# Kernel optimization log

Hardware: AMD Instinct MI355X
Metric: run time of the kernel (lower is better)

Reference implementation:

```python
import jax, jax.numpy as jnp
import numpy as np

B, S, D, H, DH = 4, 2048, 1024, 16, 64


def setup_inputs() -> dict:
    key = jax.random.key(0)
    ks = jax.random.split(key, 12)
    inp = {
        "query": jax.random.normal(ks[0], (B, S, D), jnp.float32),
        "key": jax.random.normal(ks[1], (B, S, D), jnp.float32),
        "value": jax.random.normal(ks[2], (B, S, D), jnp.float32),
        # causal mask, broadcast over batch and heads
        "mask": jnp.tril(jnp.ones((S, S), jnp.int32))[None, None, :, :],
        "Wq": jax.random.normal(ks[3], (D, D), jnp.float32) * 0.02,
        "bq": jnp.zeros((D,), jnp.float32),
        "Wk": jax.random.normal(ks[4], (D, D), jnp.float32) * 0.02,
        "bk": jnp.zeros((D,), jnp.float32),
        "Wv": jax.random.normal(ks[5], (D, D), jnp.float32) * 0.02,
        "bv": jnp.zeros((D,), jnp.float32),
        "Wo": jax.random.normal(ks[6], (D, D), jnp.float32) * 0.02,
        "bo": jnp.zeros((D,), jnp.float32),
    }
    return inp


def reference(query, key, value, mask, Wq, bq, Wk, bk, Wv, bv, Wo, bo):
    # linear projections (torch Linear: x @ W^T + b; here W stored as [in, out])
    q = query @ Wq + bq
    k = key @ Wk + bk
    v = value @ Wv + bv
    # [B, S, D] -> [B, H, S, DH]
    q = q.reshape(B, S, H, DH).transpose(0, 2, 1, 3)
    k = k.reshape(B, S, H, DH).transpose(0, 2, 1, 3)
    v = v.reshape(B, S, H, DH).transpose(0, 2, 1, 3)
    # materialized O(S^2) attention scores
    scores = jnp.einsum("bhqd,bhkd->bhqk", q, k) * (DH ** -0.5)
    scores = jnp.where(mask == 0, jnp.float32(-jnp.inf), scores)
    attn = jax.nn.softmax(scores, axis=-1)  # dropout is identity in eval
    x = jnp.einsum("bhqk,bhkd->bhqd", attn, v)
    # [B, H, S, DH] -> [B, S, D]
    x = x.transpose(0, 2, 1, 3).reshape(B, S, D)
    out = x @ Wo + bo
    return out
```

## Files before the change

kernel.cpp:

```cpp
#include <hip/hip_runtime.h>
#include <hip/hip_bf16.h>


typedef __bf16 bf16x8 __attribute__((ext_vector_type(8)));
typedef float f32x4 __attribute__((ext_vector_type(4)));

#define GLOBAL_AS __attribute__((address_space(1)))
#define LDS_AS __attribute__((address_space(3)))

#if __has_builtin(__builtin_amdgcn_exp2f)
#define EXP2(x) __builtin_amdgcn_exp2f(x)
#else
#define EXP2(x) __expf((x) * 0.6931471805599453f)
#endif
#define QSCALE 0.18033688f

static __device__ __forceinline__ unsigned short f2bf(float f) {
    __bf16 h = (__bf16)f;
    return __builtin_bit_cast(unsigned short, h);
}

static __device__ __forceinline__ void gload_lds16(const void* g, void* l) {
    __builtin_amdgcn_global_load_lds((const GLOBAL_AS void*)g, (LDS_AS void*)l, 16, 0, 0);
}

__global__ __launch_bounds__(256) void cvt3(const float* __restrict__ q,
                                            const float* __restrict__ k,
                                            const float* __restrict__ v,
                                            unsigned short* __restrict__ dq,
                                            unsigned short* __restrict__ dk,
                                            unsigned short* __restrict__ dv, int n8) {
    const int z = blockIdx.z;
    const float* src = (z == 0) ? q : (z == 1) ? k : v;
    unsigned short* dst = (z == 0) ? dq : (z == 1) ? dk : dv;
    int i = blockIdx.x * 256 + threadIdx.x;
    if (i >= n8) return;
    const float4* s = (const float4*)src + 2 * (size_t)i;
    float4 v0 = s[0], v1 = s[1];
    unsigned short h[8] = {f2bf(v0.x), f2bf(v0.y), f2bf(v0.z), f2bf(v0.w),
                           f2bf(v1.x), f2bf(v1.y), f2bf(v1.z), f2bf(v1.w)};
    *(uint4*)(dst + 8 * (size_t)i) = *(const uint4*)h;
}

__global__ void transpose_weights(const float* __restrict__ W0, const float* __restrict__ W1,
                                  const float* __restrict__ W2, const float* __restrict__ W3,
                                  unsigned short* __restrict__ T0, unsigned short* __restrict__ T1,
                                  unsigned short* __restrict__ T2, unsigned short* __restrict__ T3) {
    const float* W; unsigned short* T;
    switch (blockIdx.z) { case 0: W=W0; T=T0; break; case 1: W=W1; T=T1; break;
                          case 2: W=W2; T=T2; break; default: W=W3; T=T3; }
    __shared__ float tile[32][33];
    int tx = threadIdx.x, ty = threadIdx.y;
    int k0 = blockIdx.x * 32, n0 = blockIdx.y * 32;
#pragma unroll
    for (int j = 0; j < 4; j++) tile[ty + 8*j][tx] = W[(size_t)(k0 + ty + 8*j) * 1024 + n0 + tx];
    __syncthreads();
#pragma unroll
    for (int j = 0; j < 4; j++) T[(size_t)(n0 + ty + 8*j) * 1024 + k0 + tx] = f2bf(tile[tx][ty + 8*j]);
}

static __device__ __forceinline__ void gemm_core(const unsigned short* __restrict__ A,
                                                 const unsigned short* __restrict__ BT,
                                                 unsigned short* Asm, unsigned short* Bsm,
                                                 int rowBase, int colBase, int t,
                                                 f32x4 acc[4][4]) {
    const int lane = t & 63, w = t >> 6;
    const int g = lane >> 4, r16 = lane & 15;
    const int wr = w >> 1, wc = w & 1;
    const int K = 1024;
    const int srow = t >> 3;
    const int scol = ((t & 7) ^ ((t >> 3) & 7)) * 8;

    const unsigned short* srcA[4];
    const unsigned short* srcB[4];
#pragma unroll
    for (int j = 0; j < 4; j++) {
        srcA[j] = A  + (size_t)(rowBase + srow + 32 * j) * K + scol;
        srcB[j] = BT + (size_t)(colBase + srow + 32 * j) * K + scol;
    }
    unsigned short* dstA = Asm + 512 * w;
    unsigned short* dstB = Bsm + 512 * w;

#pragma unroll
    for (int j = 0; j < 4; j++) {
        gload_lds16(srcA[j], dstA + 2048 * j);
        gload_lds16(srcB[j], dstB + 2048 * j);
    }
    __syncthreads();

    int cur = 0;
    for (int k0 = 0; k0 < K; k0 += 64) {
        if (k0 + 64 < K) {
            unsigned short* dA = dstA + (cur ^ 1) * 8192;
            unsigned short* dB = dstB + (cur ^ 1) * 8192;
#pragma unroll
            for (int j = 0; j < 4; j++) {
                gload_lds16(srcA[j] + k0 + 64, dA + 2048 * j);
                gload_lds16(srcB[j] + k0 + 64, dB + 2048 * j);
            }
        }
        const unsigned short* As = Asm + cur * 8192;
        const unsigned short* Bs = Bsm + cur * 8192;
#pragma unroll
        for (int ks = 0; ks < 2; ks++) {
            bf16x8 a[4], b[4];
#pragma unroll
            for (int m = 0; m < 4; m++) {
                int row = 64 * wr + 16 * m + r16;
                a[m] = *(const bf16x8*)(As + row * 64 + ((4 * ks + g) ^ (row & 7)) * 8);
            }
#pragma unroll
            for (int n = 0; n < 4; n++) {
                int row = 64 * wc + 16 * n + r16;
                b[n] = *(const bf16x8*)(Bs + row * 64 + ((4 * ks + g) ^ (row & 7)) * 8);
            }
#pragma unroll
            for (int m = 0; m < 4; m++)
#pragma unroll
                for (int n = 0; n < 4; n++)
                    acc[m][n] = __builtin_amdgcn_mfma_f32_16x16x32_bf16(a[m], b[n], acc[m][n], 0, 0, 0);
        }
        __syncthreads();
        cur ^= 1;
    }
}

__global__ __launch_bounds__(256) void gemm_qkv(
        const unsigned short* __restrict__ Xq, const unsigned short* __restrict__ Xk,
        const unsigned short* __restrict__ Xv,
        const unsigned short* __restrict__ WTq, const unsigned short* __restrict__ WTk,
        const unsigned short* __restrict__ WTv,
        const float* __restrict__ bq, const float* __restrict__ bk, const float* __restrict__ bv,
        unsigned short* __restrict__ Qb, unsigned short* __restrict__ Kb,
        unsigned short* __restrict__ VT) {
    __shared__ alignas(16) unsigned short smem[32768];
    unsigned short* Asm = smem;
    unsigned short* Bsm = smem + 16384;
    const int z = blockIdx.z;
    const unsigned short* A  = (z == 0) ? Xq : (z == 1) ? Xk : Xv;
    const unsigned short* BT = (z == 0) ? WTq : (z == 1) ? WTk : WTv;
    const float* bias        = (z == 0) ? bq : (z == 1) ? bk : bv;
    const int rowBase = blockIdx.y * 128, colBase = blockIdx.x * 128;
    const int t = threadIdx.x;
    const int lane = t & 63, w = t >> 6;
    const int g = lane >> 4, r16 = lane & 15;
    const int wr = w >> 1, wc = w & 1;

    f32x4 acc[4][4] = {};
    gemm_core(A, BT, Asm, Bsm, rowBase, colBase, t, acc);

    float bv4[4];
#pragma unroll
    for (int n = 0; n < 4; n++) bv4[n] = bias[colBase + 64 * wc + 16 * n + r16];

    if (z == 2) {
        const int TS = 136;
        unsigned short* Tsm = smem;
#pragma unroll
        for (int m = 0; m < 4; m++) {
#pragma unroll
            for (int n = 0; n < 4; n++) {
                int c = 64 * wc + 16 * n + r16;
                int r = 64 * wr + 16 * m + 4 * g;
                unsigned short pk[4];
#pragma unroll
                for (int i = 0; i < 4; i++) pk[i] = f2bf(acc[m][n][i] + bv4[n]);
                *(uint2*)(Tsm + c * TS + r) = *(const uint2*)pk;
            }
        }
        __syncthreads();
        const int bidx = rowBase >> 11;
        const int sBase = rowBase & 2047;
        const int sloc = (t & 15) * 8;
#pragma unroll
        for (int jj = 0; jj < 8; jj++) {
            int dloc = (t >> 4) + 16 * jj;
            uint4 v = *(const uint4*)(Tsm + dloc * TS + sloc);
            int col = colBase + dloc;
            int hidx = col >> 6, dh = col & 63;
            *(uint4*)&VT[(((size_t)(bidx * 16 + hidx)) * 64 + dh) * 2048 + sBase + sloc] = v;
        }
    } else {
#pragma unroll
        for (int m = 0; m < 4; m++) {
#pragma unroll
            for (int n = 0; n < 4; n++) {
#pragma unroll
                for (int i = 0; i < 4; i++) {
                    int row = rowBase + 64 * wr + 16 * m + 4 * g + i;
                    int col = colBase + 64 * wc + 16 * n + r16;
                    float v = acc[m][n][i] + bv4[n];
                    int bidx = row >> 11, s = row & 2047;
                    int hidx = col >> 6, dh = col & 63;
                    size_t bh = (size_t)(bidx * 16 + hidx);
                    if (z == 0) Qb[(bh * 2048 + s) * 64 + dh] = f2bf(v * QSCALE);
                    else        Kb[(bh * 2048 + s) * 64 + dh] = f2bf(v);
                }
            }
        }
    }
}

__global__ __launch_bounds__(256) void gemm_out(const unsigned short* __restrict__ A,
                                                const unsigned short* __restrict__ BT,
                                                const float* __restrict__ bias,
                                                float* __restrict__ Out) {
    __shared__ alignas(16) unsigned short smem[32768];
    unsigned short* Asm = smem;
    unsigned short* Bsm = smem + 16384;
    const int rowBase = blockIdx.y * 128, colBase = blockIdx.x * 128;
    const int t = threadIdx.x;
    const int lane = t & 63, w = t >> 6;
    const int g = lane >> 4, r16 = lane & 15;
    const int wr = w >> 1, wc = w & 1;

    f32x4 acc[4][4] = {};
    gemm_core(A, BT, Asm, Bsm, rowBase, colBase, t, acc);

    float bv4[4];
#pragma unroll
    for (int n = 0; n < 4; n++) bv4[n] = bias[colBase + 64 * wc + 16 * n + r16];

#pragma unroll
    for (int m = 0; m < 4; m++)
#pragma unroll
        for (int n = 0; n < 4; n++)
#pragma unroll
            for (int i = 0; i < 4; i++) {
                int row = rowBase + 64 * wr + 16 * m + 4 * g + i;
                int col = colBase + 64 * wc + 16 * n + r16;
                Out[(size_t)row * 1024 + col] = acc[m][n][i] + bv4[n];
            }
}

static __device__ __forceinline__ void attn_step(
        const unsigned short* __restrict__ Ks, const unsigned short* __restrict__ Vs,
        const bf16x8 qfrag[2], f32x4 acco[4], float& m, float& lsum,
        int myq, int k0, bool diag,
        int g, int q16, int gh, int srcA, int srcB) {
    f32x4 accS[4] = {};
    __builtin_amdgcn_s_setprio(1);
#pragma unroll
    for (int ks = 0; ks < 2; ks++) {
#pragma unroll
        for (int tt = 0; tt < 4; tt++) {
            int row = 16 * tt + q16;
            bf16x8 ak = *(const bf16x8*)(Ks + row * 64 + ((4 * ks + g) ^ (row & 7)) * 8);
            accS[tt] = __builtin_amdgcn_mfma_f32_16x16x32_bf16(ak, qfrag[ks], accS[tt], 0, 0, 0);
        }
    }
    __builtin_amdgcn_s_setprio(0);

    float s[4][4];
#pragma unroll
    for (int tt = 0; tt < 4; tt++)
#pragma unroll
        for (int i = 0; i < 4; i++) {
            float v = accS[tt][i];
            if (diag) {
                int kg = k0 + 16 * tt + 4 * g + i;
                if (kg > myq) v = -1e30f;
            }
            s[tt][i] = v;
        }

    float pmax = s[0][0];
#pragma unroll
    for (int tt = 0; tt < 4; tt++)
#pragma unroll
        for (int i = 0; i < 4; i++) pmax = fmaxf(pmax, s[tt][i]);
    pmax = fmaxf(pmax, __shfl_xor(pmax, 16));
    pmax = fmaxf(pmax, __shfl_xor(pmax, 32));

    if (!__all(pmax <= m + 8.0f)) {
        float mnew = fmaxf(m, pmax);
        float sc = EXP2(m - mnew);
        lsum *= sc;
#pragma unroll
        for (int i = 0; i < 4; i++) {
            float sci = __shfl(sc, 4 * g + i);
#pragma unroll
            for (int d = 0; d < 4; d++) acco[d][i] *= sci;
        }
        m = mnew;
    }

    float tsum = 0.f;
    float p[4][4];
#pragma unroll
    for (int tt = 0; tt < 4; tt++)
#pragma unroll
        for (int i = 0; i < 4; i++) { p[tt][i] = EXP2(s[tt][i] - m); tsum += p[tt][i]; }
    tsum += __shfl_xor(tsum, 16);
    tsum += __shfl_xor(tsum, 32);
    lsum += tsum;

    unsigned lo[4], hi[4];
#pragma unroll
    for (int tt = 0; tt < 4; tt++) {
        lo[tt] = (unsigned)f2bf(p[tt][0]) | ((unsigned)f2bf(p[tt][1]) << 16);
        hi[tt] = (unsigned)f2bf(p[tt][2]) | ((unsigned)f2bf(p[tt][3]) << 16);
    }

#pragma unroll
    for (int ks = 0; ks < 2; ks++) {
        unsigned xa0 = __shfl(lo[2 * ks], srcA);
        unsigned xa1 = __shfl(hi[2 * ks], srcA);
        unsigned xa2 = __shfl(lo[2 * ks], srcB);
        unsigned xa3 = __shfl(hi[2 * ks], srcB);
        unsigned ya0 = __shfl(lo[2 * ks + 1], srcA);
        unsigned ya1 = __shfl(hi[2 * ks + 1], srcA);
        unsigned ya2 = __shfl(lo[2 * ks + 1], srcB);
        unsigned ya3 = __shfl(hi[2 * ks + 1], srcB);
        uint4 pw;
        pw.x = gh ? ya0 : xa0;
        pw.y = gh ? ya1 : xa1;
        pw.z = gh ? ya2 : xa2;
        pw.w = gh ? ya3 : xa3;
        bf16x8 pfrag = __builtin_bit_cast(bf16x8, pw);
        __builtin_amdgcn_s_setprio(1);
#pragma unroll
        for (int d = 0; d < 4; d++) {
            int row = 16 * d + q16;
            bf16x8 vv = *(const bf16x8*)(Vs + row * 64 + ((4 * ks + g) ^ (row & 7)) * 8);
            acco[d] = __builtin_amdgcn_mfma_f32_16x16x32_bf16(pfrag, vv, acco[d], 0, 0, 0);
        }
        __builtin_amdgcn_s_setprio(0);
    }
}

__global__ __launch_bounds__(256) void attn_kernel(const unsigned short* __restrict__ Q,
                                                   const unsigned short* __restrict__ Kb,
                                                   const unsigned short* __restrict__ VT,
                                                   unsigned short* __restrict__ Xout) {
    __shared__ alignas(16) unsigned short Ksm[2][4096];
    __shared__ alignas(16) unsigned short Vsm[2][4096];
    const int t = threadIdx.x;
    const int lane = t & 63, w = t >> 6;
    const int g = lane >> 4, q16 = lane & 15;
    const int bh = blockIdx.y;
    const int b = bh >> 4, h = bh & 15;

    const int srow0 = t >> 3;
    const int ssrc = ((t & 7) ^ (srow0 & 7)) * 8;
    const unsigned short* srcK[2];
    const unsigned short* srcV[2];
#pragma unroll
    for (int j = 0; j < 2; j++) {
        int row = srow0 + 32 * j;
        srcK[j] = Kb + ((size_t)bh * 2048 + row) * 64 + ssrc;
        srcV[j] = VT + ((size_t)bh * 64 + row) * 2048 + ssrc;
    }

    const int gh = g >> 1;
    const int g0 = 2 * (g & 1);
    const int srcA = 16 * g0 + q16, srcB = srcA + 16;

#pragma unroll 1
    for (int ph = 0; ph < 2; ph++) {
        const int qt = ph ? (31 - (int)blockIdx.x) : (int)blockIdx.x;
        const int q0 = qt * 64;
        const int myq = q0 + 16 * w + q16;
        const int nkt = qt + 1;

        bf16x8 qfrag[2];
        {
            const uint4* qp = (const uint4*)(Q + ((size_t)bh * 2048 + myq) * 64);
            qfrag[0] = __builtin_bit_cast(bf16x8, qp[g]);
            qfrag[1] = __builtin_bit_cast(bf16x8, qp[4 + g]);
        }

        f32x4 acco[4] = {};
        float m = -1e30f, lsum = 0.f;
        int cur = 0;

#pragma unroll
        for (int j = 0; j < 2; j++) {
            gload_lds16(srcK[j], &Ksm[0][512 * w + 2048 * j]);
            gload_lds16(srcV[j], &Vsm[0][512 * w + 2048 * j]);
        }
        __syncthreads();

        for (int kt = 0; kt < nkt; kt++) {
            if (kt + 1 < nkt) {
                int nxt = cur ^ 1;
#pragma unroll
                for (int j = 0; j < 2; j++) {
                    gload_lds16(srcK[j] + (size_t)(kt + 1) * 4096, &Ksm[nxt][512 * w + 2048 * j]);
                    gload_lds16(srcV[j] + (size_t)(kt + 1) * 64,   &Vsm[nxt][512 * w + 2048 * j]);
                }
            }
            attn_step(Ksm[cur], Vsm[cur], qfrag, acco, m, lsum,
                      myq, kt * 64, kt == nkt - 1, g, q16, gh, srcA, srcB);
            __syncthreads();
            cur ^= 1;
        }

#pragma unroll
        for (int i = 0; i < 4; i++) {
            float li = __shfl(lsum, 4 * g + i);
            float inv = 1.f / li;
            int row = q0 + 16 * w + 4 * g + i;
#pragma unroll
            for (int d = 0; d < 4; d++) {
                int col = h * 64 + 16 * d + q16;
                Xout[((size_t)b * 2048 + row) * 1024 + col] = f2bf(acco[d][i] * inv);
            }
        }
        __syncthreads();
    }
}

extern "C" void kernel_launch(void* const* d_in, const int* in_sizes, int n_in,
                              void* d_out, int out_size, void* d_ws, size_t ws_size,
                              hipStream_t stream) {
    (void)in_sizes; (void)n_in; (void)out_size; (void)ws_size;
    const float* query = (const float*)d_in[0];
    const float* key   = (const float*)d_in[1];
    const float* value = (const float*)d_in[2];
    const float* Wq = (const float*)d_in[4];
    const float* bq = (const float*)d_in[5];
    const float* Wk = (const float*)d_in[6];
    const float* bk = (const float*)d_in[7];
    const float* Wv = (const float*)d_in[8];
    const float* bv = (const float*)d_in[9];
    const float* Wo = (const float*)d_in[10];
    const float* bo = (const float*)d_in[11];

    char* base = (char*)d_ws;
    const size_t MB = 1u << 20;
    unsigned short* WTq = (unsigned short*)(base + 0 * MB);
    unsigned short* WTk = (unsigned short*)(base + 2 * MB);
    unsigned short* WTv = (unsigned short*)(base + 4 * MB);
    unsigned short* WTo = (unsigned short*)(base + 6 * MB);
    unsigned short* Qb  = (unsigned short*)(base + 8 * MB);
    unsigned short* Kbf = (unsigned short*)(base + 24 * MB);
    unsigned short* VTb = (unsigned short*)(base + 40 * MB);
    unsigned short* X   = (unsigned short*)(base + 56 * MB);

    unsigned short* Xk = (unsigned short*)d_out;
    unsigned short* Xv = Xk + (size_t)8192 * 1024;

    const int n8 = (8192 * 1024) / 8;

    transpose_weights<<<dim3(32, 32, 4), dim3(32, 8), 0, stream>>>(Wq, Wk, Wv, Wo, WTq, WTk, WTv, WTo);
    cvt3<<<dim3(4096, 1, 3), 256, 0, stream>>>(query, key, value, X, Xk, Xv, n8);
    gemm_qkv<<<dim3(8, 64, 3), 256, 0, stream>>>(X, Xk, Xv, WTq, WTk, WTv, bq, bk, bv, Qb, Kbf, VTb);
    attn_kernel<<<dim3(16, 64), 256, 0, stream>>>(Qb, Kbf, VTb, X);
    gemm_out<<<dim3(8, 64), 256, 0, stream>>>(X, WTo, bo, (float*)d_out);
}
```

Before: 344.2 us.

## Use 128-query tiles with 512-thread blocks and XCD-aware head mapping

The attention kernel now processes 128 query rows per block with 8 waves that share each K/V tile loaded into LDS, halving K/V global traffic per query row. Grid is flattened to 512 blocks with a head-index swizzle so blocks for the same (batch, head) land on the same XCD for L2 reuse. Causal pairing of query tiles is kept. Waves in the first half skip the final key tile but still wait at the barriers, which adds idle time on the diagonal, and the larger block may lower occupancy.

Result: no change. 340.7 us (-1.0%).

```diff
diff --git a/kernel.cpp b/kernel.cpp
--- a/kernel.cpp
+++ b/kernel.cpp
@@ -329,7 +329,7 @@
     }
 }
 
-__global__ __launch_bounds__(256) void attn_kernel(const unsigned short* __restrict__ Q,
+__global__ __launch_bounds__(512) void attn_kernel(const unsigned short* __restrict__ Q,
                                                    const unsigned short* __restrict__ Kb,
                                                    const unsigned short* __restrict__ VT,
                                                    unsigned short* __restrict__ Xout) {
@@ -338,19 +338,15 @@
     const int t = threadIdx.x;
     const int lane = t & 63, w = t >> 6;
     const int g = lane >> 4, q16 = lane & 15;
-    const int bh = blockIdx.y;
+    const unsigned wgid = blockIdx.x;
+    const int bh = 8 * (wgid & 7) + ((wgid >> 3) & 7);
+    const int qp = wgid >> 6;
     const int b = bh >> 4, h = bh & 15;
 
-    const int srow0 = t >> 3;
-    const int ssrc = ((t & 7) ^ (srow0 & 7)) * 8;
-    const unsigned short* srcK[2];
-    const unsigned short* srcV[2];
-#pragma unroll
-    for (int j = 0; j < 2; j++) {
-        int row = srow0 + 32 * j;
-        srcK[j] = Kb + ((size_t)bh * 2048 + row) * 64 + ssrc;
-        srcV[j] = VT + ((size_t)bh * 64 + row) * 2048 + ssrc;
-    }
+    const int srow = t >> 3;
+    const int ssrc = ((t & 7) ^ (srow & 7)) * 8;
+    const unsigned short* srcK = Kb + ((size_t)bh * 2048 + srow) * 64 + ssrc;
+    const unsigned short* srcV = VT + ((size_t)bh * 64 + srow) * 2048 + ssrc;
 
     const int gh = g >> 1;
     const int g0 = 2 * (g & 1);
@@ -358,40 +354,35 @@
 
 #pragma unroll 1
     for (int ph = 0; ph < 2; ph++) {
-        const int qt = ph ? (31 - (int)blockIdx.x) : (int)blockIdx.x;
-        const int q0 = qt * 64;
-        const int myq = q0 + 16 * w + q16;
-        const int nkt = qt + 1;
+        const int qt128 = ph ? (15 - qp) : qp;
+        const int myq = qt128 * 128 + 16 * w + q16;
+        const int nkt = 2 * qt128 + 2;
+        const int diagKt = 2 * qt128 + (w >> 2);
 
         bf16x8 qfrag[2];
         {
-            const uint4* qp = (const uint4*)(Q + ((size_t)bh * 2048 + myq) * 64);
-            qfrag[0] = __builtin_bit_cast(bf16x8, qp[g]);
-            qfrag[1] = __builtin_bit_cast(bf16x8, qp[4 + g]);
+            const uint4* qp_ = (const uint4*)(Q + ((size_t)bh * 2048 + myq) * 64);
+            qfrag[0] = __builtin_bit_cast(bf16x8, qp_[g]);
+            qfrag[1] = __builtin_bit_cast(bf16x8, qp_[4 + g]);
         }
 
         f32x4 acco[4] = {};
         float m = -1e30f, lsum = 0.f;
         int cur = 0;
 
-#pragma unroll
-        for (int j = 0; j < 2; j++) {
-            gload_lds16(srcK[j], &Ksm[0][512 * w + 2048 * j]);
-            gload_lds16(srcV[j], &Vsm[0][512 * w + 2048 * j]);
-        }
+        gload_lds16(srcK, &Ksm[0][512 * w]);
+        gload_lds16(srcV, &Vsm[0][512 * w]);
         __syncthreads();
 
         for (int kt = 0; kt < nkt; kt++) {
             if (kt + 1 < nkt) {
                 int nxt = cur ^ 1;
-#pragma unroll
-                for (int j = 0; j < 2; j++) {
-                    gload_lds16(srcK[j] + (size_t)(kt + 1) * 4096, &Ksm[nxt][512 * w + 2048 * j]);
-                    gload_lds16(srcV[j] + (size_t)(kt + 1) * 64,   &Vsm[nxt][512 * w + 2048 * j]);
-                }
-            }
-            attn_step(Ksm[cur], Vsm[cur], qfrag, acco, m, lsum,
-                      myq, kt * 64, kt == nkt - 1, g, q16, gh, srcA, srcB);
+                gload_lds16(srcK + (size_t)(kt + 1) * 4096, &Ksm[nxt][512 * w]);
+                gload_lds16(srcV + (size_t)(kt + 1) * 64,   &Vsm[nxt][512 * w]);
+            }
+            if (kt <= diagKt)
+                attn_step(Ksm[cur], Vsm[cur], qfrag, acco, m, lsum,
+                          myq, kt * 64, kt == diagKt, g, q16, gh, srcA, srcB);
             __syncthreads();
             cur ^= 1;
         }
@@ -400,7 +391,7 @@
         for (int i = 0; i < 4; i++) {
             float li = __shfl(lsum, 4 * g + i);
             float inv = 1.f / li;
-            int row = q0 + 16 * w + 4 * g + i;
+            int row = qt128 * 128 + 16 * w + 4 * g + i;
 #pragma unroll
             for (int d = 0; d < 4; d++) {
                 int col = h * 64 + 16 * d + q16;
@@ -446,6 +437,6 @@
     transpose_weights<<<dim3(32, 32, 4), dim3(32, 8), 0, stream>>>(Wq, Wk, Wv, Wo, WTq, WTk, WTv, WTo);
     cvt3<<<dim3(4096, 1, 3), 256, 0, stream>>>(query, key, value, X, Xk, Xv, n8);
     gemm_qkv<<<dim3(8, 64, 3), 256, 0, stream>>>(X, Xk, Xv, WTq, WTk, WTv, bq, bk, bv, Qb, Kbf, VTb);
-    attn_kernel<<<dim3(16, 64), 256, 0, stream>>>(Qb, Kbf, VTb, X);
+    attn_kernel<<<512, 512, 0, stream>>>(Qb, Kbf, VTb, X);
     gemm_out<<<dim3(8, 64), 256, 0, stream>>>(X, WTo, bo, (float*)d_out);
 }
```
